# Optimization experiments

Measured on AMD Instinct MI355X. Metric: run time of the kernel, lower is better.

## Reference

```python
import jax, jax.numpy as jnp
import numpy as np
from jax import lax

PRE_NMS_TOPN = 2000
POST_NMS_TOPN = 1000
NMS_THRESH = 0.7
MIN_BOX_SIZE = 4.0
BBOX_XFORM_CLIP = 4.135  # log(1000/16), standard clamp on dw/dh


def setup_inputs() -> dict:
    key = jax.random.key(0)
    k1, k2, k3, k4 = jax.random.split(key, 4)
    B, N = 8, 250000
    H, W = 800, 1333
    rpn_bbox_pred = jax.random.normal(k1, (B, N, 4), jnp.float32) * 0.5
    objectness = jax.random.normal(k2, (B, N), jnp.float32)
    # realistic anchors: centers inside image, sizes in [16, 256]
    ctr = jax.random.uniform(k3, (N, 2), jnp.float32) * jnp.array([W, H], jnp.float32)
    wh = jax.random.uniform(k4, (N, 2), jnp.float32) * 240.0 + 16.0
    anchors = jnp.concatenate([ctr - 0.5 * wh, ctr + 0.5 * wh], axis=-1)
    return {"rpn_bbox_pred": rpn_bbox_pred, "objectness": objectness,
            "anchors": anchors, "height": H, "width": W}


def _decode_clip(anchors, deltas, height, width):
    # anchors (1,N,4) broadcast against deltas (B,N,4); boxes are x1,y1,x2,y2
    aw = anchors[..., 2] - anchors[..., 0]
    ah = anchors[..., 3] - anchors[..., 1]
    ax = anchors[..., 0] + 0.5 * aw
    ay = anchors[..., 1] + 0.5 * ah
    dx, dy = deltas[..., 0], deltas[..., 1]
    dw = jnp.minimum(deltas[..., 2], BBOX_XFORM_CLIP)
    dh = jnp.minimum(deltas[..., 3], BBOX_XFORM_CLIP)
    px = dx * aw + ax
    py = dy * ah + ay
    pw = jnp.exp(dw) * aw
    ph = jnp.exp(dh) * ah
    x1 = jnp.clip(px - 0.5 * pw, 0.0, float(width))
    y1 = jnp.clip(py - 0.5 * ph, 0.0, float(height))
    x2 = jnp.clip(px + 0.5 * pw, 0.0, float(width))
    y2 = jnp.clip(py + 0.5 * ph, 0.0, float(height))
    return jnp.stack([x1, y1, x2, y2], axis=-1)


def _pairwise_iou(boxes):
    # boxes (K,4) -> iou (K,K)
    x1, y1, x2, y2 = boxes[:, 0], boxes[:, 1], boxes[:, 2], boxes[:, 3]
    area = (x2 - x1) * (y2 - y1)
    iw = jnp.maximum(jnp.minimum(x2[:, None], x2[None, :]) - jnp.maximum(x1[:, None], x1[None, :]), 0.0)
    ih = jnp.maximum(jnp.minimum(y2[:, None], y2[None, :]) - jnp.maximum(y1[:, None], y1[None, :]), 0.0)
    inter = iw * ih
    return inter / (area[:, None] + area[None, :] - inter + 1e-9)


def _nms_keep(boxes, valid):
    # sequential greedy NMS over score-sorted boxes (K,4); returns keep mask (K,)
    iou = lax.stop_gradient(_pairwise_iou(boxes))
    idxs = jnp.arange(PRE_NMS_TOPN)
    def body(i, keep):
        sup = (iou[i] > NMS_THRESH) & keep[i] & (idxs > i)
        return keep & (~sup)
    return lax.fori_loop(0, PRE_NMS_TOPN, body, valid)


def _per_image(boxes, scores):
    # boxes (N,4), scores (N,)
    ws = boxes[:, 2] - boxes[:, 0]
    hs = boxes[:, 3] - boxes[:, 1]
    size_ok = (ws >= MIN_BOX_SIZE) & (hs >= MIN_BOX_SIZE)
    masked = jnp.where(size_ok, scores, -jnp.inf)
    top_s, order = lax.top_k(masked, PRE_NMS_TOPN)   # descending sort + pre-NMS topN
    top_boxes = boxes[order]                          # (PRE,4)
    valid = top_s > -jnp.inf                          # boxes surviving size filter
    keep = _nms_keep(top_boxes, valid)
    # take first POST_NMS_TOPN kept boxes in score order (fixed-shape padding)
    sel = jnp.sort(jnp.where(keep, jnp.arange(PRE_NMS_TOPN), PRE_NMS_TOPN))[:POST_NMS_TOPN]
    out_valid = sel < PRE_NMS_TOPN
    sel_c = jnp.minimum(sel, PRE_NMS_TOPN - 1)
    out = jnp.where(out_valid[:, None], top_boxes[sel_c], 0.0)
    return out, out_valid


def reference(rpn_bbox_pred, objectness, anchors, height, width):
    proposals = _decode_clip(anchors[None], rpn_bbox_pred, height, width)  # (B,N,4)
    out, valid = jax.vmap(_per_image)(proposals, objectness)
    # padded equivalent of the ragged per-image list: (B,POST,4) boxes + (B,POST) validity
    return out, valid
```

## Files before the change

### kernel.cpp

```cpp
#include <hip/hip_runtime.h>
#include <hip/hip_bf16.h>

#define NBUCK 8192
#define P1B   32
#define CAP   4096
#define TOPN  2000
#define NP2   2048
#define OUTN  1000
#define NST   64
#define NSLOT 8
#define SLOTW 2048

typedef unsigned int u32x4 __attribute__((ext_vector_type(4)));
typedef __attribute__((address_space(1))) const unsigned GUP;
typedef __attribute__((address_space(3))) unsigned LUP;

__device__ __forceinline__ float4 decode_box(const float4 a, const float4 d, float W, float H) {
    float aw = a.z - a.x;
    float ah = a.w - a.y;
    float ax = a.x + 0.5f * aw;
    float ay = a.y + 0.5f * ah;
    float dw = fminf(d.z, 4.135f);
    float dh = fminf(d.w, 4.135f);
    float px = d.x * aw + ax;
    float py = d.y * ah + ay;
    float pw = expf(dw) * aw;
    float ph = expf(dh) * ah;
    float4 r;
    r.x = fminf(fmaxf(px - 0.5f * pw, 0.0f), W);
    r.y = fminf(fmaxf(py - 0.5f * ph, 0.0f), H);
    r.z = fminf(fmaxf(px + 0.5f * pw, 0.0f), W);
    r.w = fminf(fmaxf(py + 0.5f * ph, 0.0f), H);
    return r;
}

__device__ __forceinline__ unsigned score_key(const float4 a, const float4 d, float W, float H, float s) {
    float4 b = decode_box(a, d, W, H);
    bool ok = ((b.z - b.x) >= 4.0f) && ((b.w - b.y) >= 4.0f);
    float ms = ok ? s : -INFINITY;
    unsigned u = __float_as_uint(ms);
    return (u & 0x80000000u) ? ~u : (u | 0x80000000u);
}

__global__ void __launch_bounds__(1024) k_pass1(const float* __restrict__ pred,
        const float* __restrict__ obj, const float* __restrict__ anch,
        const int* __restrict__ Hp, const int* __restrict__ Wp,
        unsigned* __restrict__ keys, unsigned* __restrict__ hist,
        unsigned* __restrict__ cnt, unsigned* __restrict__ remInit, int N) {
    __shared__ unsigned h[2 * NBUCK];
    int t = threadIdx.x;
    int b = blockIdx.y, g = blockIdx.x;
    if (g == 0 && t < 64) { if (t == 0) cnt[b * 64] = 0; remInit[b * 64 + t] = 0; }
    for (int i = t; i < 2 * NBUCK; i += 1024) h[i] = 0;
    __syncthreads();
    int chunk = (N + P1B - 1) / P1B;
    int base = g * chunk;
    int end = base + chunk; if (end > N) end = N;
    float W = (float)*Wp, H = (float)*Hp;
    unsigned cp = (t & 1) ? NBUCK : 0;
    for (int n = base + t; n < end; n += 1024) {
        float4 a = ((const float4*)anch)[n];
        float4 d = ((const float4*)pred)[(size_t)b * N + n];
        float s = obj[(size_t)b * N + n];
        unsigned key = score_key(a, d, W, H, s);
        keys[(size_t)b * N + n] = key;
        atomicAdd(&h[cp + (key >> 19)], 1u);
    }
    __syncthreads();
    for (int i = t; i < NBUCK; i += 1024) {
        unsigned v = h[i] + h[NBUCK + i];
        if (v) atomicAdd(&hist[b * NBUCK + i], v);
    }
}

__global__ void k_scan(const unsigned* __restrict__ hist, unsigned* __restrict__ Lb) {
    __shared__ unsigned h[NBUCK];
    __shared__ unsigned csum[256];
    __shared__ unsigned suf[256];
    __shared__ int tcS;
    __shared__ unsigned beforeS;
    int b = blockIdx.x, t = threadIdx.x;
    const unsigned* src = hist + (size_t)b * NBUCK;
    for (int i = t * 4; i < NBUCK; i += 1024) {
        uint4 v = *(const uint4*)(src + i);
        h[i] = v.x; h[i + 1] = v.y; h[i + 2] = v.z; h[i + 3] = v.w;
    }
    if (t == 0) tcS = -1;
    __syncthreads();
    unsigned s = 0;
    for (int j = 0; j < 32; j++) s += h[t * 32 + j];
    csum[t] = s; suf[t] = s;
    __syncthreads();
    for (int d = 1; d < 256; d <<= 1) {
        unsigned v = (t + d < 256) ? suf[t + d] : 0;
        __syncthreads();
        suf[t] += v;
        __syncthreads();
    }
    if (suf[t] >= (unsigned)TOPN && (t == 255 || suf[t + 1] < (unsigned)TOPN)) {
        tcS = t; beforeS = (t == 255) ? 0u : suf[t + 1];
    }
    __syncthreads();
    if (t == 0) {
        unsigned L = 0;
        int tc = tcS;
        if (tc >= 0) {
            unsigned r = beforeS;
            for (int bkt = tc * 32 + 31;; bkt--) {
                r += h[bkt];
                if (r >= (unsigned)TOPN || bkt == tc * 32) { L = (unsigned)bkt; break; }
            }
        }
        Lb[b] = L;
    }
}

__global__ void k_collect(const unsigned* __restrict__ keys, const unsigned* __restrict__ Lb,
                          unsigned* __restrict__ count, unsigned long long* __restrict__ cand,
                          int N) {
    __shared__ unsigned lk[1024], ln[1024];
    __shared__ unsigned lcnt, lbase;
    int b = blockIdx.y, t = threadIdx.x;
    if (t == 0) lcnt = 0;
    __syncthreads();
    unsigned L = Lb[b];
    const unsigned* kb = keys + (size_t)b * N;
    int e = blockIdx.x * 256 + t;
    int n0 = e * 4;
    if (n0 + 3 < N) {
        uint4 kv = ((const uint4*)kb)[e];
        if ((kv.x >> 19) >= L) { unsigned p = atomicAdd(&lcnt, 1u); lk[p] = kv.x; ln[p] = n0; }
        if ((kv.y >> 19) >= L) { unsigned p = atomicAdd(&lcnt, 1u); lk[p] = kv.y; ln[p] = n0 + 1; }
        if ((kv.z >> 19) >= L) { unsigned p = atomicAdd(&lcnt, 1u); lk[p] = kv.z; ln[p] = n0 + 2; }
        if ((kv.w >> 19) >= L) { unsigned p = atomicAdd(&lcnt, 1u); lk[p] = kv.w; ln[p] = n0 + 3; }
    } else {
        for (int j = 0; j < 4; j++) {
            int n = n0 + j;
            if (n < N) {
                unsigned k = kb[n];
                if ((k >> 19) >= L) { unsigned p = atomicAdd(&lcnt, 1u); lk[p] = k; ln[p] = n; }
            }
        }
    }
    __syncthreads();
    if (t == 0) lbase = atomicAdd(&count[b * 64], lcnt);
    __syncthreads();
    unsigned c = lcnt, bs = lbase;
    for (unsigned i = t; i < c; i += 256) {
        unsigned pos = bs + i;
        if (pos < CAP) cand[(size_t)b * CAP + pos] =
            ((unsigned long long)lk[i] << 32) | (unsigned)(~ln[i]);
    }
}

#define REGX(e, p, d, lo)  ((lo) == (d) ? ((e) >= (p) ? (e) : (p)) : ((e) >= (p) ? (p) : (e)))

__global__ void __launch_bounds__(256) k_sort1(unsigned long long* __restrict__ cand,
        const unsigned* __restrict__ count) {
    __shared__ unsigned long long s[512];
    int b = blockIdx.x >> 3, g = blockIdx.x & 7;
    int t = threadIdx.x;
    unsigned cnt = count[b * 64]; if (cnt > CAP) cnt = CAP;
    unsigned long long* cb = cand + (size_t)b * CAP + g * 512;
    int g0 = g * 512 + t, g1 = g * 512 + t + 256;
    unsigned long long e0 = (g0 < (int)cnt) ? cb[t] : 0ULL;
    unsigned long long e1 = (g1 < (int)cnt) ? cb[t + 256] : 0ULL;

    #pragma unroll
    for (int k = 2; k <= 64; k <<= 1) {
        bool d0 = ((g0 & k) == 0);
        bool d1 = ((g1 & k) == 0);
        #pragma unroll
        for (int j = k >> 1; j >= 1; j >>= 1) {
            bool lo = ((t & j) == 0);
            unsigned long long p0 = __shfl_xor(e0, j, 64);
            unsigned long long p1 = __shfl_xor(e1, j, 64);
            e0 = REGX(e0, p0, d0, lo);
            e1 = REGX(e1, p1, d1, lo);
        }
    }
    for (int k = 128; k <= 512; k <<= 1) {
        s[t] = e0; s[t + 256] = e1;
        __syncthreads();
        for (int j = k >> 1; j >= 64; j >>= 1) {
            int i = ((t & ~(j - 1)) << 1) | (t & (j - 1));
            int l = i + j;
            bool desc = (((g * 512 + i) & k) == 0);
            unsigned long long x = s[i], y = s[l];
            if (desc ? (x < y) : (x > y)) { s[i] = y; s[l] = x; }
            __syncthreads();
        }
        e0 = s[t]; e1 = s[t + 256];
        bool d0 = ((g0 & k) == 0);
        bool d1 = ((g1 & k) == 0);
        #pragma unroll
        for (int j = 32; j >= 1; j >>= 1) {
            bool lo = ((t & j) == 0);
            unsigned long long p0 = __shfl_xor(e0, j, 64);
            unsigned long long p1 = __shfl_xor(e1, j, 64);
            e0 = REGX(e0, p0, d0, lo);
            e1 = REGX(e1, p1, d1, lo);
        }
    }
    cb[t] = e0; cb[t + 256] = e1;
}

__global__ void __launch_bounds__(1024) k_sort2(const unsigned long long* __restrict__ cand,
        const float* __restrict__ pred, const float* __restrict__ anch,
        const int* __restrict__ Hp, const int* __restrict__ Wp,
        float4* __restrict__ topbox, unsigned* __restrict__ remInit, int N) {
    __shared__ unsigned long long s[CAP];
    int b = blockIdx.x, t = threadIdx.x;
    const unsigned long long* cb = cand + (size_t)b * CAP;
    unsigned long long e0 = cb[t], e1 = cb[t + 1024], e2 = cb[t + 2048], e3 = cb[t + 3072];
    for (int k = 1024; k <= 4096; k <<= 1) {
        s[t] = e0; s[t + 1024] = e1; s[t + 2048] = e2; s[t + 3072] = e3;
        __syncthreads();
        for (int j = k >> 1; j >= 64; j >>= 1) {
            #pragma unroll
            for (int cc = 0; cc < 2; cc++) {
                int c = t + cc * 1024;
                int i = ((c & ~(j - 1)) << 1) | (c & (j - 1));
                int l = i + j;
                bool desc = ((i & k) == 0);
                unsigned long long x = s[i], y = s[l];
                if (desc ? (x < y) : (x > y)) { s[i] = y; s[l] = x; }
            }
            __syncthreads();
        }
        e0 = s[t]; e1 = s[t + 1024]; e2 = s[t + 2048]; e3 = s[t + 3072];
        bool d0 = ((t & k) == 0);
        bool d1 = (((t + 1024) & k) == 0);
        bool d2 = (((t + 2048) & k) == 0);
        bool d3 = (((t + 3072) & k) == 0);
        #pragma unroll
        for (int j = 32; j >= 1; j >>= 1) {
            bool lo = ((t & j) == 0);
            unsigned long long p0 = __shfl_xor(e0, j, 64);
            unsigned long long p1 = __shfl_xor(e1, j, 64);
            unsigned long long p2 = __shfl_xor(e2, j, 64);
            unsigned long long p3 = __shfl_xor(e3, j, 64);
            e0 = REGX(e0, p0, d0, lo);
            e1 = REGX(e1, p1, d1, lo);
            e2 = REGX(e2, p2, d2, lo);
            e3 = REGX(e3, p3, d3, lo);
        }
    }
    float W = (float)*Wp, H = (float)*Hp;
    #pragma unroll
    for (int m = 0; m < 2; m++) {
        unsigned long long v = m ? e1 : e0;
        int r = t + m * 1024;
        unsigned key = (unsigned)(v >> 32);
        bool valid = key > 0x007FFFFFu;
        float4 outb = {0.f, 0.f, 0.f, 0.f};
        if (valid) {
            unsigned idx = ~((unsigned)v);
            float4 a = ((const float4*)anch)[idx];
            float4 d = ((const float4*)pred)[(size_t)b * N + idx];
            outb = decode_box(a, d, W, H);
        }
        topbox[(size_t)b * NP2 + r] = outb;
        if (r < TOPN && !valid) atomicOr(&remInit[b * 64 + (r >> 5)], 1u << (r & 31));
    }
}

__global__ void __launch_bounds__(256) k_mask(const float4* __restrict__ topbox,
                                              unsigned* __restrict__ maskT) {
    const double MID = 23488103.0 / 33554432.0;
    __shared__ float4 bx[NP2];
    __shared__ float ar[NP2];
    int b = blockIdx.y, c = blockIdx.x;
    int t = threadIdx.x;
    int j0 = c * 32;
    for (int i = j0 + t; i < NP2; i += 256) {
        float4 v = topbox[(size_t)b * NP2 + i];
        bx[i] = v;
        ar[i] = (v.z - v.x) * (v.w - v.y);
    }
    __syncthreads();
    int r = t & 31;
    int wg = t >> 5;
    int i = j0 + r;
    float4 bi = bx[i];
    float areai = ar[i];
    unsigned* outc = maskT + ((size_t)(b * NST + c)) * SLOTW;
    for (int w = wg; w < c; w += 8) outc[w * 32 + r] = 0u;
    for (int w = c + wg; w < 64; w += 8) {
        unsigned bits = 0;
        int jbase = w * 32;
        #pragma unroll
        for (int jj = 0; jj < 32; jj++) {
            int j = jbase + jj;
            float4 bj = bx[j];
            float iw = fmaxf(fminf(bi.z, bj.z) - fmaxf(bi.x, bj.x), 0.0f);
            float ih = fmaxf(fminf(bi.w, bj.w) - fmaxf(bi.y, bj.y), 0.0f);
            float inter = iw * ih;
            float denom = areai + ar[j] - inter + 1e-9f;
            if ((double)inter >= MID * (double)denom) bits |= (1u << jj);
        }
        if (w == c) bits &= ~((2u << r) - 1u);
        outc[w * 32 + r] = bits;
    }
}

__global__ void __launch_bounds__(512) k_nms(const unsigned* __restrict__ maskT,
        const unsigned* __restrict__ remInit, const float4* __restrict__ topbox,
        float* __restrict__ out, int B) {
    __shared__ __align__(16) unsigned smbuf[NSLOT * SLOTW];
    __shared__ int ready[NST];
    __shared__ int consumed;
    __shared__ int stop;
    int b = blockIdx.x;
    int t = threadIdx.x;
    const unsigned* m = maskT + (size_t)b * NST * SLOTW;

    float4* ob = (float4*)out + (size_t)b * OUTN;
    for (int i = t; i < OUTN; i += 512) ob[i] = make_float4(0.f, 0.f, 0.f, 0.f);
    float* vout = out + (size_t)B * (OUTN * 4) + (size_t)b * OUTN;
    for (int i = t; i < OUTN; i += 512) vout[i] = 0.0f;

    if (t < NST) ready[t] = 0;
    if (t == 0) { consumed = 0; stop = 0; }
    __syncthreads();

    unsigned removed = 0xFFFFFFFFu;

    if (t >= 64) {
        int w = t >> 6;
        int lam = t & 63;
        int base = ((lam >> 3) << 5) + ((((lam & 7) ^ ((lam >> 3) & 7))) << 2);
        #pragma unroll 1
        for (int s = w - 1; s < NST; s += 7) {
            if (__hip_atomic_load(&stop, __ATOMIC_RELAXED, __HIP_MEMORY_SCOPE_WORKGROUP)) break;
            while (__hip_atomic_load(&consumed, __ATOMIC_ACQUIRE,
                   __HIP_MEMORY_SCOPE_WORKGROUP) < s - (NSLOT - 1))
                __builtin_amdgcn_s_sleep(2);
            const unsigned* gs = m + (size_t)s * SLOTW + base;
            unsigned* sl = smbuf + (s & (NSLOT - 1)) * SLOTW;
            #pragma unroll
            for (int i = 0; i < 8; i++)
                __builtin_amdgcn_global_load_lds((GUP*)(gs + i * 256),
                                                 (LUP*)(sl + i * 256), 16, 0, 0);
            asm volatile("s_waitcnt vmcnt(0)" ::: "memory");
            if (lam == 0) __hip_atomic_store(&ready[s], 1, __ATOMIC_RELEASE,
                                             __HIP_MEMORY_SCOPE_WORKGROUP);
        }
    } else {
        removed = remInit[b * 64 + t];
        if (t == 62) removed |= 0xFFFF0000u;
        if (t == 63) removed = 0xFFFFFFFFu;
        int e = t & 7;
        int keptRun = 0;
        #pragma unroll 1
        for (int s = 0; s < NST; s++) {
            while (!__hip_atomic_load(&ready[s], __ATOMIC_ACQUIRE,
                   __HIP_MEMORY_SCOPE_WORKGROUP))
                __builtin_amdgcn_s_sleep(2);
            const u32x4* sq = (const u32x4*)(smbuf + (s & (NSLOT - 1)) * SLOTW) + t * 8;
            unsigned R[32];
            #pragma unroll
            for (int k = 0; k < 8; k++) *(u32x4*)&R[k << 2] = sq[k ^ e];
            __builtin_amdgcn_sched_group_barrier(0x100, 8, 0);
            unsigned alive = ~__builtin_amdgcn_readlane(removed, s);
            unsigned Is[32];
            #pragma unroll
            for (int q = 0; q < 32; q++) Is[q] = __builtin_amdgcn_readlane(R[q], s);
            #pragma unroll
            for (int q = 0; q < 32; q++) alive &= ~(((alive >> q) & 1u) ? Is[q] : 0u);
            unsigned a0 = 0, a1 = 0, a2 = 0, a3 = 0;
            #pragma unroll
            for (int q = 0; q < 32; q += 4) {
                a0 |= ((alive >> q) & 1u)       ? R[q]     : 0u;
                a1 |= ((alive >> (q + 1)) & 1u) ? R[q + 1] : 0u;
                a2 |= ((alive >> (q + 2)) & 1u) ? R[q + 2] : 0u;
                a3 |= ((alive >> (q + 3)) & 1u) ? R[q + 3] : 0u;
            }
            removed |= (a0 | a1) | (a2 | a3);
            keptRun += __popc(~__builtin_amdgcn_readlane(removed, s));
            if (keptRun >= OUTN) {
                if (t == 0) {
                    __hip_atomic_store(&stop, 1, __ATOMIC_RELAXED, __HIP_MEMORY_SCOPE_WORKGROUP);
                    __hip_atomic_store(&consumed, NST, __ATOMIC_RELEASE, __HIP_MEMORY_SCOPE_WORKGROUP);
                }
                break;
            }
            if (t == 0) __hip_atomic_store(&consumed, s + 1, __ATOMIC_RELEASE,
                                           __HIP_MEMORY_SCOPE_WORKGROUP);
        }
        unsigned keep = ~removed;
        int cnt = __popc(keep);
        int ex = cnt;
        for (int off = 1; off < 64; off <<= 1) {
            int v = __shfl_up(ex, off, 64);
            if (t >= off) ex += v;
        }
        ex -= cnt;
        int pos = ex;
        for (int j = 0; j < 32; j++) {
            if ((keep >> j) & 1u) {
                if (pos < OUTN) {
                    float4 bxv = topbox[(size_t)b * NP2 + t * 32 + j];
                    ob[pos] = bxv;
                    vout[pos] = 1.0f;
                }
                pos++;
            }
        }
    }
}

extern "C" void kernel_launch(void* const* d_in, const int* in_sizes, int n_in,
                              void* d_out, int out_size, void* d_ws, size_t ws_size,
                              hipStream_t stream) {
    const float* pred = (const float*)d_in[0];
    const float* obj  = (const float*)d_in[1];
    const float* anch = (const float*)d_in[2];
    const int* Hp = (const int*)d_in[3];
    const int* Wp = (const int*)d_in[4];
    int N = in_sizes[2] / 4;
    int B = in_sizes[1] / N;

    char* ws = (char*)d_ws;
    size_t off = 0;
    auto take = [&](size_t bytes) { void* p = ws + off; off = (off + bytes + 255) & ~(size_t)255; return p; };

    size_t regA_bytes = (size_t)B * N * 4;
    size_t mask_bytes = (size_t)B * NST * SLOTW * 4;
    char* regA = (char*)take(regA_bytes > mask_bytes ? regA_bytes : mask_bytes);
    unsigned* keys  = (unsigned*)regA;
    unsigned* maskT = (unsigned*)regA;
    unsigned* hist           = (unsigned*)take((size_t)B * NBUCK * 4);
    unsigned long long* cand = (unsigned long long*)take((size_t)B * CAP * 8);
    float4* topbox           = (float4*)take((size_t)B * NP2 * 16);
    unsigned* cnt            = (unsigned*)take((size_t)B * 64 * 4);
    unsigned* Lb             = (unsigned*)take((size_t)B * 64 * 4);
    unsigned* remInit        = (unsigned*)take((size_t)B * 64 * 4);

    hipMemsetAsync(hist, 0, (size_t)B * NBUCK * 4, stream);

    k_pass1  <<<dim3(P1B, B), 1024, 0, stream>>>(pred, obj, anch, Hp, Wp, keys, hist, cnt, remInit, N);
    k_scan   <<<B, 256, 0, stream>>>(hist, Lb);
    k_collect<<<dim3((N + 1023) / 1024, B), 256, 0, stream>>>(keys, Lb, cnt, cand, N);
    k_sort1  <<<B * 8, 256, 0, stream>>>(cand, cnt);
    k_sort2  <<<B, 1024, 0, stream>>>(cand, pred, anch, Hp, Wp, topbox, remInit, N);
    k_mask   <<<dim3(NST, B), 256, 0, stream>>>(topbox, maskT);
    k_nms    <<<B, 512, 0, stream>>>(maskT, remInit, topbox, (float*)d_out, B);
}
```

Measured before the change: 123.4 us.

## Fuse all pipeline stages into one persistent kernel with software grid barriers

Replaces the seven separate kernel launches (plus memset) with one persistent kernel of 240 blocks. The blocks step through histogram, threshold scan, collect, two sort stages, mask build and NMS, separated by atomic-counter grid barriers. A small zeroing kernel replaces the memset and also clears the counters, remInit and barrier state. The aim is to remove launch and inter-kernel gap overhead. The cost is that many stages leave most blocks idle, the barrier relies on all 240 blocks being co-resident, and the mask stage now keeps 32 of 64 row words per block per pass.

After: 288.9 us. +134.1%, slower.

```diff
diff --git a/kernel.cpp b/kernel.cpp
--- a/kernel.cpp
+++ b/kernel.cpp
@@ -2,7 +2,8 @@
 #include <hip/hip_bf16.h>
 
 #define NBUCK 8192
-#define P1B   32
+#define NBLK  240
+#define PIMG  30
 #define CAP   4096
 #define TOPN  2000
 #define NP2   2048
@@ -10,6 +11,7 @@
 #define NST   64
 #define NSLOT 8
 #define SLOTW 2048
+#define ZWORDS (2*NBUCK*4 + 512 + 512 + 64)
 
 typedef unsigned int u32x4 __attribute__((ext_vector_type(4)));
 typedef __attribute__((address_space(1))) const unsigned GUP;
@@ -42,369 +44,417 @@
     return (u & 0x80000000u) ? ~u : (u | 0x80000000u);
 }
 
-__global__ void __launch_bounds__(1024) k_pass1(const float* __restrict__ pred,
-        const float* __restrict__ obj, const float* __restrict__ anch,
-        const int* __restrict__ Hp, const int* __restrict__ Wp,
-        unsigned* __restrict__ keys, unsigned* __restrict__ hist,
-        unsigned* __restrict__ cnt, unsigned* __restrict__ remInit, int N) {
-    __shared__ unsigned h[2 * NBUCK];
+__global__ void k_zero(unsigned* __restrict__ p, int nq) {
+    int i = blockIdx.x * 256 + threadIdx.x;
+    if (i < nq) ((u32x4*)p)[i] = (u32x4){0u, 0u, 0u, 0u};
+}
+
+__device__ __forceinline__ void gridbar(unsigned* bar, int cell) {
+    __syncthreads();
+    if (threadIdx.x == 0) {
+        unsigned* c = bar + cell * 2;
+        unsigned* g = bar + cell * 2 + 1;
+        __threadfence();
+        unsigned g0 = __hip_atomic_load(g, __ATOMIC_RELAXED, __HIP_MEMORY_SCOPE_AGENT);
+        unsigned a = __hip_atomic_fetch_add(c, 1u, __ATOMIC_ACQ_REL, __HIP_MEMORY_SCOPE_AGENT);
+        if (a == NBLK - 1) {
+            __hip_atomic_store(c, 0u, __ATOMIC_RELAXED, __HIP_MEMORY_SCOPE_AGENT);
+            __hip_atomic_store(g, g0 + 1u, __ATOMIC_RELEASE, __HIP_MEMORY_SCOPE_AGENT);
+        } else {
+            while (__hip_atomic_load(g, __ATOMIC_ACQUIRE, __HIP_MEMORY_SCOPE_AGENT) == g0)
+                __builtin_amdgcn_s_sleep(8);
+        }
+        __threadfence();
+    }
+    __syncthreads();
+}
+
+#define REGX(e, p, d, lo)  ((lo) == (d) ? ((e) >= (p) ? (e) : (p)) : ((e) >= (p) ? (p) : (e)))
+
+__global__ void __launch_bounds__(1024) k_mega(
+        const float* __restrict__ pred, const float* __restrict__ obj,
+        const float* __restrict__ anch, const int* __restrict__ Hp,
+        const int* __restrict__ Wp, unsigned* __restrict__ keys,
+        unsigned* __restrict__ hist, unsigned* __restrict__ cntg,
+        unsigned* __restrict__ remInit, unsigned* __restrict__ Lb,
+        unsigned long long* __restrict__ cand, float4* __restrict__ topbox,
+        unsigned* __restrict__ maskT, float* __restrict__ out,
+        unsigned* __restrict__ bar, int N, int B) {
+    __shared__ __align__(16) char Lraw[65808];
+    int bid = blockIdx.x;
     int t = threadIdx.x;
-    int b = blockIdx.y, g = blockIdx.x;
-    if (g == 0 && t < 64) { if (t == 0) cnt[b * 64] = 0; remInit[b * 64 + t] = 0; }
-    for (int i = t; i < 2 * NBUCK; i += 1024) h[i] = 0;
-    __syncthreads();
-    int chunk = (N + P1B - 1) / P1B;
-    int base = g * chunk;
-    int end = base + chunk; if (end > N) end = N;
     float W = (float)*Wp, H = (float)*Hp;
-    unsigned cp = (t & 1) ? NBUCK : 0;
-    for (int n = base + t; n < end; n += 1024) {
-        float4 a = ((const float4*)anch)[n];
-        float4 d = ((const float4*)pred)[(size_t)b * N + n];
-        float s = obj[(size_t)b * N + n];
-        unsigned key = score_key(a, d, W, H, s);
-        keys[(size_t)b * N + n] = key;
-        atomicAdd(&h[cp + (key >> 19)], 1u);
-    }
-    __syncthreads();
-    for (int i = t; i < NBUCK; i += 1024) {
-        unsigned v = h[i] + h[NBUCK + i];
-        if (v) atomicAdd(&hist[b * NBUCK + i], v);
-    }
-}
-
-__global__ void k_scan(const unsigned* __restrict__ hist, unsigned* __restrict__ Lb) {
-    __shared__ unsigned h[NBUCK];
-    __shared__ unsigned csum[256];
-    __shared__ unsigned suf[256];
-    __shared__ int tcS;
-    __shared__ unsigned beforeS;
-    int b = blockIdx.x, t = threadIdx.x;
-    const unsigned* src = hist + (size_t)b * NBUCK;
-    for (int i = t * 4; i < NBUCK; i += 1024) {
-        uint4 v = *(const uint4*)(src + i);
-        h[i] = v.x; h[i + 1] = v.y; h[i + 2] = v.z; h[i + 3] = v.w;
-    }
-    if (t == 0) tcS = -1;
-    __syncthreads();
-    unsigned s = 0;
-    for (int j = 0; j < 32; j++) s += h[t * 32 + j];
-    csum[t] = s; suf[t] = s;
-    __syncthreads();
-    for (int d = 1; d < 256; d <<= 1) {
-        unsigned v = (t + d < 256) ? suf[t + d] : 0;
-        __syncthreads();
-        suf[t] += v;
-        __syncthreads();
-    }
-    if (suf[t] >= (unsigned)TOPN && (t == 255 || suf[t + 1] < (unsigned)TOPN)) {
-        tcS = t; beforeS = (t == 255) ? 0u : suf[t + 1];
-    }
-    __syncthreads();
-    if (t == 0) {
-        unsigned L = 0;
-        int tc = tcS;
-        if (tc >= 0) {
-            unsigned r = beforeS;
-            for (int bkt = tc * 32 + 31;; bkt--) {
-                r += h[bkt];
-                if (r >= (unsigned)TOPN || bkt == tc * 32) { L = (unsigned)bkt; break; }
-            }
-        }
-        Lb[b] = L;
-    }
-}
-
-__global__ void k_collect(const unsigned* __restrict__ keys, const unsigned* __restrict__ Lb,
-                          unsigned* __restrict__ count, unsigned long long* __restrict__ cand,
-                          int N) {
-    __shared__ unsigned lk[1024], ln[1024];
-    __shared__ unsigned lcnt, lbase;
-    int b = blockIdx.y, t = threadIdx.x;
-    if (t == 0) lcnt = 0;
-    __syncthreads();
-    unsigned L = Lb[b];
-    const unsigned* kb = keys + (size_t)b * N;
-    int e = blockIdx.x * 256 + t;
-    int n0 = e * 4;
-    if (n0 + 3 < N) {
-        uint4 kv = ((const uint4*)kb)[e];
-        if ((kv.x >> 19) >= L) { unsigned p = atomicAdd(&lcnt, 1u); lk[p] = kv.x; ln[p] = n0; }
-        if ((kv.y >> 19) >= L) { unsigned p = atomicAdd(&lcnt, 1u); lk[p] = kv.y; ln[p] = n0 + 1; }
-        if ((kv.z >> 19) >= L) { unsigned p = atomicAdd(&lcnt, 1u); lk[p] = kv.z; ln[p] = n0 + 2; }
-        if ((kv.w >> 19) >= L) { unsigned p = atomicAdd(&lcnt, 1u); lk[p] = kv.w; ln[p] = n0 + 3; }
-    } else {
-        for (int j = 0; j < 4; j++) {
-            int n = n0 + j;
-            if (n < N) {
-                unsigned k = kb[n];
-                if ((k >> 19) >= L) { unsigned p = atomicAdd(&lcnt, 1u); lk[p] = k; ln[p] = n; }
-            }
-        }
-    }
-    __syncthreads();
-    if (t == 0) lbase = atomicAdd(&count[b * 64], lcnt);
-    __syncthreads();
-    unsigned c = lcnt, bs = lbase;
-    for (unsigned i = t; i < c; i += 256) {
-        unsigned pos = bs + i;
-        if (pos < CAP) cand[(size_t)b * CAP + pos] =
-            ((unsigned long long)lk[i] << 32) | (unsigned)(~ln[i]);
-    }
-}
-
-#define REGX(e, p, d, lo)  ((lo) == (d) ? ((e) >= (p) ? (e) : (p)) : ((e) >= (p) ? (p) : (e)))
-
-__global__ void __launch_bounds__(256) k_sort1(unsigned long long* __restrict__ cand,
-        const unsigned* __restrict__ count) {
-    __shared__ unsigned long long s[512];
-    int b = blockIdx.x >> 3, g = blockIdx.x & 7;
-    int t = threadIdx.x;
-    unsigned cnt = count[b * 64]; if (cnt > CAP) cnt = CAP;
-    unsigned long long* cb = cand + (size_t)b * CAP + g * 512;
-    int g0 = g * 512 + t, g1 = g * 512 + t + 256;
-    unsigned long long e0 = (g0 < (int)cnt) ? cb[t] : 0ULL;
-    unsigned long long e1 = (g1 < (int)cnt) ? cb[t + 256] : 0ULL;
-
-    #pragma unroll
-    for (int k = 2; k <= 64; k <<= 1) {
-        bool d0 = ((g0 & k) == 0);
-        bool d1 = ((g1 & k) == 0);
+
+    {
+        unsigned* h = (unsigned*)Lraw;
+        int b = bid / PIMG, g = bid % PIMG;
+        for (int i = t; i < 2 * NBUCK; i += 1024) h[i] = 0;
+        __syncthreads();
+        int chunk = (N + PIMG - 1) / PIMG;
+        int base = g * chunk;
+        int end = base + chunk; if (end > N) end = N;
+        unsigned cp = (t & 1) ? NBUCK : 0;
+        for (int n = base + t; n < end; n += 1024) {
+            float4 a = ((const float4*)anch)[n];
+            float4 d = ((const float4*)pred)[(size_t)b * N + n];
+            float s = obj[(size_t)b * N + n];
+            unsigned key = score_key(a, d, W, H, s);
+            keys[(size_t)b * N + n] = key;
+            atomicAdd(&h[cp + (key >> 19)], 1u);
+        }
+        __syncthreads();
+        for (int i = t; i < NBUCK; i += 1024) {
+            unsigned v = h[i] + h[NBUCK + i];
+            if (v) atomicAdd(&hist[b * NBUCK + i], v);
+        }
+    }
+    gridbar(bar, 0);
+
+    if (bid < B) {
+        unsigned* h1   = (unsigned*)Lraw;
+        unsigned* csum = (unsigned*)(Lraw + 32768);
+        unsigned* suf  = (unsigned*)(Lraw + 33792);
+        int* tcS       = (int*)(Lraw + 34816);
+        unsigned* befS = (unsigned*)(Lraw + 34820);
+        int b = bid;
+        const unsigned* src = hist + (size_t)b * NBUCK;
+        for (int i = t * 4; i < NBUCK; i += 4096) {
+            uint4 v = *(const uint4*)(src + i);
+            h1[i] = v.x; h1[i + 1] = v.y; h1[i + 2] = v.z; h1[i + 3] = v.w;
+        }
+        if (t == 0) *tcS = -1;
+        __syncthreads();
+        if (t < 256) {
+            unsigned s = 0;
+            for (int j = 0; j < 32; j++) s += h1[t * 32 + j];
+            csum[t] = s; suf[t] = s;
+        }
+        __syncthreads();
+        for (int d = 1; d < 256; d <<= 1) {
+            unsigned v = (t < 256 && t + d < 256) ? suf[t + d] : 0;
+            __syncthreads();
+            if (t < 256) suf[t] += v;
+            __syncthreads();
+        }
+        if (t < 256 && suf[t] >= (unsigned)TOPN && (t == 255 || suf[t + 1] < (unsigned)TOPN)) {
+            *tcS = t; *befS = (t == 255) ? 0u : suf[t + 1];
+        }
+        __syncthreads();
+        if (t == 0) {
+            unsigned L = 0;
+            int tc = *tcS;
+            if (tc >= 0) {
+                unsigned r = *befS;
+                for (int bkt = tc * 32 + 31;; bkt--) {
+                    r += h1[bkt];
+                    if (r >= (unsigned)TOPN || bkt == tc * 32) { L = (unsigned)bkt; break; }
+                }
+            }
+            Lb[b] = L;
+        }
+    }
+    gridbar(bar, 1);
+
+    {
+        unsigned* lk    = (unsigned*)Lraw;
+        unsigned* ln    = (unsigned*)(Lraw + 16384);
+        unsigned* lcnt  = (unsigned*)(Lraw + 32768);
+        unsigned* lbase = (unsigned*)(Lraw + 32784);
+        int b = bid / PIMG, g = bid % PIMG;
+        int grp = t >> 8, lt = t & 255;
+        const unsigned* kb = keys + (size_t)b * N;
+        unsigned Lth = Lb[b];
+        int V = N >> 2;
+        int SUBT = (V + 255) >> 8;
+        for (int it = 0; it < 3; it++) {
+            int st = g * 4 + grp + (PIMG * 4) * it;
+            if (lt == 0) lcnt[grp] = 0;
+            __syncthreads();
+            bool act = st < SUBT;
+            if (act) {
+                int e = st * 256 + lt;
+                if (e < V) {
+                    uint4 kv = ((const uint4*)kb)[e];
+                    int n0 = e * 4;
+                    if ((kv.x >> 19) >= Lth) { unsigned p = atomicAdd(&lcnt[grp], 1u); lk[grp * 1024 + p] = kv.x; ln[grp * 1024 + p] = n0; }
+                    if ((kv.y >> 19) >= Lth) { unsigned p = atomicAdd(&lcnt[grp], 1u); lk[grp * 1024 + p] = kv.y; ln[grp * 1024 + p] = n0 + 1; }
+                    if ((kv.z >> 19) >= Lth) { unsigned p = atomicAdd(&lcnt[grp], 1u); lk[grp * 1024 + p] = kv.z; ln[grp * 1024 + p] = n0 + 2; }
+                    if ((kv.w >> 19) >= Lth) { unsigned p = atomicAdd(&lcnt[grp], 1u); lk[grp * 1024 + p] = kv.w; ln[grp * 1024 + p] = n0 + 3; }
+                }
+            }
+            __syncthreads();
+            if (act && lt == 0) lbase[grp] = atomicAdd(&cntg[b * 64], lcnt[grp]);
+            __syncthreads();
+            if (act) {
+                unsigned c2 = lcnt[grp], bs = lbase[grp];
+                for (unsigned i2 = lt; i2 < c2; i2 += 256) {
+                    unsigned pos = bs + i2;
+                    if (pos < CAP) cand[(size_t)b * CAP + pos] =
+                        ((unsigned long long)lk[grp * 1024 + i2] << 32) | (unsigned)(~ln[grp * 1024 + i2]);
+                }
+            }
+            __syncthreads();
+        }
+    }
+    gridbar(bar, 2);
+
+    if (bid < 64) {
+        unsigned long long* s1 = (unsigned long long*)Lraw;
+        int b = bid >> 3, g = bid & 7;
+        unsigned cnt = cntg[b * 64]; if (cnt > CAP) cnt = CAP;
+        unsigned long long* cb = cand + (size_t)b * CAP + g * 512;
+        int g0 = g * 512 + t, g1 = g * 512 + t + 256;
+        unsigned long long e0 = 0, e1 = 0;
+        if (t < 256) {
+            e0 = (g0 < (int)cnt) ? cb[t] : 0ULL;
+            e1 = (g1 < (int)cnt) ? cb[t + 256] : 0ULL;
+            #pragma unroll
+            for (int k = 2; k <= 64; k <<= 1) {
+                bool d0 = ((g0 & k) == 0);
+                bool d1 = ((g1 & k) == 0);
+                #pragma unroll
+                for (int j = k >> 1; j >= 1; j >>= 1) {
+                    bool lo = ((t & j) == 0);
+                    unsigned long long p0 = __shfl_xor(e0, j, 64);
+                    unsigned long long p1 = __shfl_xor(e1, j, 64);
+                    e0 = REGX(e0, p0, d0, lo);
+                    e1 = REGX(e1, p1, d1, lo);
+                }
+            }
+        }
+        for (int k = 128; k <= 512; k <<= 1) {
+            if (t < 256) { s1[t] = e0; s1[t + 256] = e1; }
+            __syncthreads();
+            for (int j = k >> 1; j >= 64; j >>= 1) {
+                if (t < 256) {
+                    int i = ((t & ~(j - 1)) << 1) | (t & (j - 1));
+                    int l = i + j;
+                    bool desc = (((g * 512 + i) & k) == 0);
+                    unsigned long long x = s1[i], y = s1[l];
+                    if (desc ? (x < y) : (x > y)) { s1[i] = y; s1[l] = x; }
+                }
+                __syncthreads();
+            }
+            if (t < 256) {
+                e0 = s1[t]; e1 = s1[t + 256];
+                bool d0 = ((g0 & k) == 0);
+                bool d1 = ((g1 & k) == 0);
+                #pragma unroll
+                for (int j = 32; j >= 1; j >>= 1) {
+                    bool lo = ((t & j) == 0);
+                    unsigned long long p0 = __shfl_xor(e0, j, 64);
+                    unsigned long long p1 = __shfl_xor(e1, j, 64);
+                    e0 = REGX(e0, p0, d0, lo);
+                    e1 = REGX(e1, p1, d1, lo);
+                }
+            }
+        }
+        if (t < 256) { cb[t] = e0; cb[t + 256] = e1; }
+    }
+    gridbar(bar, 3);
+
+    if (bid < B) {
+        unsigned long long* s = (unsigned long long*)Lraw;
+        int b = bid;
+        const unsigned long long* cb = cand + (size_t)b * CAP;
+        unsigned long long e0 = cb[t], e1 = cb[t + 1024], e2 = cb[t + 2048], e3 = cb[t + 3072];
+        for (int k = 1024; k <= 4096; k <<= 1) {
+            s[t] = e0; s[t + 1024] = e1; s[t + 2048] = e2; s[t + 3072] = e3;
+            __syncthreads();
+            for (int j = k >> 1; j >= 64; j >>= 1) {
+                #pragma unroll
+                for (int cc = 0; cc < 2; cc++) {
+                    int c = t + cc * 1024;
+                    int i = ((c & ~(j - 1)) << 1) | (c & (j - 1));
+                    int l = i + j;
+                    bool desc = ((i & k) == 0);
+                    unsigned long long x = s[i], y = s[l];
+                    if (desc ? (x < y) : (x > y)) { s[i] = y; s[l] = x; }
+                }
+                __syncthreads();
+            }
+            e0 = s[t]; e1 = s[t + 1024]; e2 = s[t + 2048]; e3 = s[t + 3072];
+            bool d0 = ((t & k) == 0);
+            bool d1 = (((t + 1024) & k) == 0);
+            bool d2 = (((t + 2048) & k) == 0);
+            bool d3 = (((t + 3072) & k) == 0);
+            #pragma unroll
+            for (int j = 32; j >= 1; j >>= 1) {
+                bool lo = ((t & j) == 0);
+                unsigned long long p0 = __shfl_xor(e0, j, 64);
+                unsigned long long p1 = __shfl_xor(e1, j, 64);
+                unsigned long long p2 = __shfl_xor(e2, j, 64);
+                unsigned long long p3 = __shfl_xor(e3, j, 64);
+                e0 = REGX(e0, p0, d0, lo);
+                e1 = REGX(e1, p1, d1, lo);
+                e2 = REGX(e2, p2, d2, lo);
+                e3 = REGX(e3, p3, d3, lo);
+            }
+        }
         #pragma unroll
-        for (int j = k >> 1; j >= 1; j >>= 1) {
-            bool lo = ((t & j) == 0);
-            unsigned long long p0 = __shfl_xor(e0, j, 64);
-            unsigned long long p1 = __shfl_xor(e1, j, 64);
-            e0 = REGX(e0, p0, d0, lo);
-            e1 = REGX(e1, p1, d1, lo);
-        }
-    }
-    for (int k = 128; k <= 512; k <<= 1) {
-        s[t] = e0; s[t + 256] = e1;
-        __syncthreads();
-        for (int j = k >> 1; j >= 64; j >>= 1) {
-            int i = ((t & ~(j - 1)) << 1) | (t & (j - 1));
-            int l = i + j;
-            bool desc = (((g * 512 + i) & k) == 0);
-            unsigned long long x = s[i], y = s[l];
-            if (desc ? (x < y) : (x > y)) { s[i] = y; s[l] = x; }
-            __syncthreads();
-        }
-        e0 = s[t]; e1 = s[t + 256];
-        bool d0 = ((g0 & k) == 0);
-        bool d1 = ((g1 & k) == 0);
-        #pragma unroll
-        for (int j = 32; j >= 1; j >>= 1) {
-            bool lo = ((t & j) == 0);
-            unsigned long long p0 = __shfl_xor(e0, j, 64);
-            unsigned long long p1 = __shfl_xor(e1, j, 64);
-            e0 = REGX(e0, p0, d0, lo);
-            e1 = REGX(e1, p1, d1, lo);
-        }
-    }
-    cb[t] = e0; cb[t + 256] = e1;
-}
-
-__global__ void __launch_bounds__(1024) k_sort2(const unsigned long long* __restrict__ cand,
-        const float* __restrict__ pred, const float* __restrict__ anch,
-        const int* __restrict__ Hp, const int* __restrict__ Wp,
-        float4* __restrict__ topbox, unsigned* __restrict__ remInit, int N) {
-    __shared__ unsigned long long s[CAP];
-    int b = blockIdx.x, t = threadIdx.x;
-    const unsigned long long* cb = cand + (size_t)b * CAP;
-    unsigned long long e0 = cb[t], e1 = cb[t + 1024], e2 = cb[t + 2048], e3 = cb[t + 3072];
-    for (int k = 1024; k <= 4096; k <<= 1) {
-        s[t] = e0; s[t + 1024] = e1; s[t + 2048] = e2; s[t + 3072] = e3;
-        __syncthreads();
-        for (int j = k >> 1; j >= 64; j >>= 1) {
-            #pragma unroll
-            for (int cc = 0; cc < 2; cc++) {
-                int c = t + cc * 1024;
-                int i = ((c & ~(j - 1)) << 1) | (c & (j - 1));
-                int l = i + j;
-                bool desc = ((i & k) == 0);
-                unsigned long long x = s[i], y = s[l];
-                if (desc ? (x < y) : (x > y)) { s[i] = y; s[l] = x; }
-            }
-            __syncthreads();
-        }
-        e0 = s[t]; e1 = s[t + 1024]; e2 = s[t + 2048]; e3 = s[t + 3072];
-        bool d0 = ((t & k) == 0);
-        bool d1 = (((t + 1024) & k) == 0);
-        bool d2 = (((t + 2048) & k) == 0);
-        bool d3 = (((t + 3072) & k) == 0);
-        #pragma unroll
-        for (int j = 32; j >= 1; j >>= 1) {
-            bool lo = ((t & j) == 0);
-            unsigned long long p0 = __shfl_xor(e0, j, 64);
-            unsigned long long p1 = __shfl_xor(e1, j, 64);
-            unsigned long long p2 = __shfl_xor(e2, j, 64);
-            unsigned long long p3 = __shfl_xor(e3, j, 64);
-            e0 = REGX(e0, p0, d0, lo);
-            e1 = REGX(e1, p1, d1, lo);
-            e2 = REGX(e2, p2, d2, lo);
-            e3 = REGX(e3, p3, d3, lo);
-        }
-    }
-    float W = (float)*Wp, H = (float)*Hp;
-    #pragma unroll
-    for (int m = 0; m < 2; m++) {
-        unsigned long long v = m ? e1 : e0;
-        int r = t + m * 1024;
-        unsigned key = (unsigned)(v >> 32);
-        bool valid = key > 0x007FFFFFu;
-        float4 outb = {0.f, 0.f, 0.f, 0.f};
-        if (valid) {
-            unsigned idx = ~((unsigned)v);
-            float4 a = ((const float4*)anch)[idx];
-            float4 d = ((const float4*)pred)[(size_t)b * N + idx];
-            outb = decode_box(a, d, W, H);
-        }
-        topbox[(size_t)b * NP2 + r] = outb;
-        if (r < TOPN && !valid) atomicOr(&remInit[b * 64 + (r >> 5)], 1u << (r & 31));
-    }
-}
-
-__global__ void __launch_bounds__(256) k_mask(const float4* __restrict__ topbox,
-                                              unsigned* __restrict__ maskT) {
-    const double MID = 23488103.0 / 33554432.0;
-    __shared__ float4 bx[NP2];
-    __shared__ float ar[NP2];
-    int b = blockIdx.y, c = blockIdx.x;
-    int t = threadIdx.x;
-    int j0 = c * 32;
-    for (int i = j0 + t; i < NP2; i += 256) {
-        float4 v = topbox[(size_t)b * NP2 + i];
-        bx[i] = v;
-        ar[i] = (v.z - v.x) * (v.w - v.y);
-    }
-    __syncthreads();
-    int r = t & 31;
-    int wg = t >> 5;
-    int i = j0 + r;
-    float4 bi = bx[i];
-    float areai = ar[i];
-    unsigned* outc = maskT + ((size_t)(b * NST + c)) * SLOTW;
-    for (int w = wg; w < c; w += 8) outc[w * 32 + r] = 0u;
-    for (int w = c + wg; w < 64; w += 8) {
-        unsigned bits = 0;
-        int jbase = w * 32;
-        #pragma unroll
-        for (int jj = 0; jj < 32; jj++) {
-            int j = jbase + jj;
-            float4 bj = bx[j];
-            float iw = fmaxf(fminf(bi.z, bj.z) - fmaxf(bi.x, bj.x), 0.0f);
-            float ih = fmaxf(fminf(bi.w, bj.w) - fmaxf(bi.y, bj.y), 0.0f);
-            float inter = iw * ih;
-            float denom = areai + ar[j] - inter + 1e-9f;
-            if ((double)inter >= MID * (double)denom) bits |= (1u << jj);
-        }
-        if (w == c) bits &= ~((2u << r) - 1u);
-        outc[w * 32 + r] = bits;
-    }
-}
-
-__global__ void __launch_bounds__(512) k_nms(const unsigned* __restrict__ maskT,
-        const unsigned* __restrict__ remInit, const float4* __restrict__ topbox,
-        float* __restrict__ out, int B) {
-    __shared__ __align__(16) unsigned smbuf[NSLOT * SLOTW];
-    __shared__ int ready[NST];
-    __shared__ int consumed;
-    __shared__ int stop;
-    int b = blockIdx.x;
-    int t = threadIdx.x;
-    const unsigned* m = maskT + (size_t)b * NST * SLOTW;
-
-    float4* ob = (float4*)out + (size_t)b * OUTN;
-    for (int i = t; i < OUTN; i += 512) ob[i] = make_float4(0.f, 0.f, 0.f, 0.f);
-    float* vout = out + (size_t)B * (OUTN * 4) + (size_t)b * OUTN;
-    for (int i = t; i < OUTN; i += 512) vout[i] = 0.0f;
-
-    if (t < NST) ready[t] = 0;
-    if (t == 0) { consumed = 0; stop = 0; }
-    __syncthreads();
-
-    unsigned removed = 0xFFFFFFFFu;
-
-    if (t >= 64) {
-        int w = t >> 6;
-        int lam = t & 63;
-        int base = ((lam >> 3) << 5) + ((((lam & 7) ^ ((lam >> 3) & 7))) << 2);
-        #pragma unroll 1
-        for (int s = w - 1; s < NST; s += 7) {
-            if (__hip_atomic_load(&stop, __ATOMIC_RELAXED, __HIP_MEMORY_SCOPE_WORKGROUP)) break;
-            while (__hip_atomic_load(&consumed, __ATOMIC_ACQUIRE,
-                   __HIP_MEMORY_SCOPE_WORKGROUP) < s - (NSLOT - 1))
-                __builtin_amdgcn_s_sleep(2);
-            const unsigned* gs = m + (size_t)s * SLOTW + base;
-            unsigned* sl = smbuf + (s & (NSLOT - 1)) * SLOTW;
-            #pragma unroll
-            for (int i = 0; i < 8; i++)
-                __builtin_amdgcn_global_load_lds((GUP*)(gs + i * 256),
-                                                 (LUP*)(sl + i * 256), 16, 0, 0);
-            asm volatile("s_waitcnt vmcnt(0)" ::: "memory");
-            if (lam == 0) __hip_atomic_store(&ready[s], 1, __ATOMIC_RELEASE,
-                                             __HIP_MEMORY_SCOPE_WORKGROUP);
-        }
-    } else {
-        removed = remInit[b * 64 + t];
-        if (t == 62) removed |= 0xFFFF0000u;
-        if (t == 63) removed = 0xFFFFFFFFu;
-        int e = t & 7;
-        int keptRun = 0;
-        #pragma unroll 1
-        for (int s = 0; s < NST; s++) {
-            while (!__hip_atomic_load(&ready[s], __ATOMIC_ACQUIRE,
-                   __HIP_MEMORY_SCOPE_WORKGROUP))
-                __builtin_amdgcn_s_sleep(2);
-            const u32x4* sq = (const u32x4*)(smbuf + (s & (NSLOT - 1)) * SLOTW) + t * 8;
-            unsigned R[32];
-            #pragma unroll
-            for (int k = 0; k < 8; k++) *(u32x4*)&R[k << 2] = sq[k ^ e];
-            __builtin_amdgcn_sched_group_barrier(0x100, 8, 0);
-            unsigned alive = ~__builtin_amdgcn_readlane(removed, s);
-            unsigned Is[32];
-            #pragma unroll
-            for (int q = 0; q < 32; q++) Is[q] = __builtin_amdgcn_readlane(R[q], s);
-            #pragma unroll
-            for (int q = 0; q < 32; q++) alive &= ~(((alive >> q) & 1u) ? Is[q] : 0u);
-            unsigned a0 = 0, a1 = 0, a2 = 0, a3 = 0;
-            #pragma unroll
-            for (int q = 0; q < 32; q += 4) {
-                a0 |= ((alive >> q) & 1u)       ? R[q]     : 0u;
-                a1 |= ((alive >> (q + 1)) & 1u) ? R[q + 1] : 0u;
-                a2 |= ((alive >> (q + 2)) & 1u) ? R[q + 2] : 0u;
-                a3 |= ((alive >> (q + 3)) & 1u) ? R[q + 3] : 0u;
-            }
-            removed |= (a0 | a1) | (a2 | a3);
-            keptRun += __popc(~__builtin_amdgcn_readlane(removed, s));
-            if (keptRun >= OUTN) {
-                if (t == 0) {
-                    __hip_atomic_store(&stop, 1, __ATOMIC_RELAXED, __HIP_MEMORY_SCOPE_WORKGROUP);
-                    __hip_atomic_store(&consumed, NST, __ATOMIC_RELEASE, __HIP_MEMORY_SCOPE_WORKGROUP);
-                }
-                break;
-            }
-            if (t == 0) __hip_atomic_store(&consumed, s + 1, __ATOMIC_RELEASE,
-                                           __HIP_MEMORY_SCOPE_WORKGROUP);
-        }
-        unsigned keep = ~removed;
-        int cnt = __popc(keep);
-        int ex = cnt;
-        for (int off = 1; off < 64; off <<= 1) {
-            int v = __shfl_up(ex, off, 64);
-            if (t >= off) ex += v;
-        }
-        ex -= cnt;
-        int pos = ex;
-        for (int j = 0; j < 32; j++) {
-            if ((keep >> j) & 1u) {
-                if (pos < OUTN) {
-                    float4 bxv = topbox[(size_t)b * NP2 + t * 32 + j];
-                    ob[pos] = bxv;
-                    vout[pos] = 1.0f;
-                }
-                pos++;
+        for (int m = 0; m < 2; m++) {
+            unsigned long long v = m ? e1 : e0;
+            int r = t + m * 1024;
+            unsigned key = (unsigned)(v >> 32);
+            bool valid = key > 0x007FFFFFu;
+            float4 outb = {0.f, 0.f, 0.f, 0.f};
+            if (valid) {
+                unsigned idx = ~((unsigned)v);
+                float4 a = ((const float4*)anch)[idx];
+                float4 d = ((const float4*)pred)[(size_t)b * N + idx];
+                outb = decode_box(a, d, W, H);
+            }
+            topbox[(size_t)b * NP2 + r] = outb;
+            if (r < TOPN && !valid) atomicOr(&remInit[b * 64 + (r >> 5)], 1u << (r & 31));
+        }
+    }
+    gridbar(bar, 4);
+
+    {
+        const double MID = 23488103.0 / 33554432.0;
+        float4* bx = (float4*)Lraw;
+        float*  ar = (float*)(Lraw + 32768);
+        for (int it = 0; it < 3; it++) {
+            int task = bid + it * NBLK;
+            bool act = task < 8 * NST;
+            int mb = task >> 6, c = task & 63;
+            int j0 = c * 32;
+            if (act) {
+                for (int i = j0 + t; i < NP2; i += 1024) {
+                    float4 v = topbox[(size_t)mb * NP2 + i];
+                    bx[i] = v;
+                    ar[i] = (v.z - v.x) * (v.w - v.y);
+                }
+            }
+            __syncthreads();
+            if (act) {
+                int r = t & 31;
+                int wg = t >> 5;
+                int i = j0 + r;
+                float4 bi = bx[i];
+                float areai = ar[i];
+                unsigned* outc = maskT + ((size_t)(mb * NST + c)) * SLOTW;
+                for (int w = wg; w < 64; w += 32) {
+                    if (w < c) { outc[w * 32 + r] = 0u; continue; }
+                    unsigned bits = 0;
+                    int jbase = w * 32;
+                    #pragma unroll
+                    for (int jj = 0; jj < 32; jj++) {
+                        int j = jbase + jj;
+                        float4 bj = bx[j];
+                        float iw = fmaxf(fminf(bi.z, bj.z) - fmaxf(bi.x, bj.x), 0.0f);
+                        float ih = fmaxf(fminf(bi.w, bj.w) - fmaxf(bi.y, bj.y), 0.0f);
+                        float inter = iw * ih;
+                        float denom = areai + ar[j] - inter + 1e-9f;
+                        if ((double)inter >= MID * (double)denom) bits |= (1u << jj);
+                    }
+                    if (w == c) bits &= ~((2u << r) - 1u);
+                    outc[w * 32 + r] = bits;
+                }
+            }
+            __syncthreads();
+        }
+    }
+    gridbar(bar, 5);
+
+    if (bid < B) {
+        unsigned* smbuf = (unsigned*)Lraw;
+        int* ready      = (int*)(Lraw + 65536);
+        int* consumed   = (int*)(Lraw + 65792);
+        int* stop       = (int*)(Lraw + 65796);
+        int b = bid;
+        const unsigned* m = maskT + (size_t)b * NST * SLOTW;
+
+        float4* ob = (float4*)out + (size_t)b * OUTN;
+        for (int i = t; i < OUTN; i += 1024) ob[i] = make_float4(0.f, 0.f, 0.f, 0.f);
+        float* vout = out + (size_t)B * (OUTN * 4) + (size_t)b * OUTN;
+        for (int i = t; i < OUTN; i += 1024) vout[i] = 0.0f;
+
+        if (t < NST) ready[t] = 0;
+        if (t == 0) { *consumed = 0; *stop = 0; }
+        __syncthreads();
+
+        if (t >= 512) {
+        } else if (t >= 64) {
+            int w = t >> 6;
+            int lam = t & 63;
+            int base = ((lam >> 3) << 5) + ((((lam & 7) ^ ((lam >> 3) & 7))) << 2);
+            #pragma unroll 1
+            for (int s = w - 1; s < NST; s += 7) {
+                if (__hip_atomic_load(stop, __ATOMIC_RELAXED, __HIP_MEMORY_SCOPE_WORKGROUP)) break;
+                while (__hip_atomic_load(consumed, __ATOMIC_ACQUIRE,
+                       __HIP_MEMORY_SCOPE_WORKGROUP) < s - (NSLOT - 1))
+                    __builtin_amdgcn_s_sleep(2);
+                const unsigned* gs = m + (size_t)s * SLOTW + base;
+                unsigned* sl = smbuf + (s & (NSLOT - 1)) * SLOTW;
+                #pragma unroll
+                for (int i = 0; i < 8; i++)
+                    __builtin_amdgcn_global_load_lds((GUP*)(gs + i * 256),
+                                                     (LUP*)(sl + i * 256), 16, 0, 0);
+                asm volatile("s_waitcnt vmcnt(0)" ::: "memory");
+                if (lam == 0) __hip_atomic_store(&ready[s], 1, __ATOMIC_RELEASE,
+                                                 __HIP_MEMORY_SCOPE_WORKGROUP);
+            }
+        } else {
+            unsigned removed = remInit[b * 64 + t];
+            if (t == 62) removed |= 0xFFFF0000u;
+            if (t == 63) removed = 0xFFFFFFFFu;
+            int e = t & 7;
+            int keptRun = 0;
+            #pragma unroll 1
+            for (int s = 0; s < NST; s++) {
+                while (!__hip_atomic_load(&ready[s], __ATOMIC_ACQUIRE,
+                       __HIP_MEMORY_SCOPE_WORKGROUP))
+                    __builtin_amdgcn_s_sleep(2);
+                const u32x4* sq = (const u32x4*)(smbuf + (s & (NSLOT - 1)) * SLOTW) + t * 8;
+                unsigned R[32];
+                #pragma unroll
+                for (int k = 0; k < 8; k++) *(u32x4*)&R[k << 2] = sq[k ^ e];
+                __builtin_amdgcn_sched_group_barrier(0x100, 8, 0);
+                unsigned alive = ~__builtin_amdgcn_readlane(removed, s);
+                unsigned Is[32];
+                #pragma unroll
+                for (int q = 0; q < 32; q++) Is[q] = __builtin_amdgcn_readlane(R[q], s);
+                #pragma unroll
+                for (int q = 0; q < 32; q++) alive &= ~(((alive >> q) & 1u) ? Is[q] : 0u);
+                unsigned a0 = 0, a1 = 0, a2 = 0, a3 = 0;
+                #pragma unroll
+                for (int q = 0; q < 32; q += 4) {
+                    a0 |= ((alive >> q) & 1u)       ? R[q]     : 0u;
+                    a1 |= ((alive >> (q + 1)) & 1u) ? R[q + 1] : 0u;
+                    a2 |= ((alive >> (q + 2)) & 1u) ? R[q + 2] : 0u;
+                    a3 |= ((alive >> (q + 3)) & 1u) ? R[q + 3] : 0u;
+                }
+                removed |= (a0 | a1) | (a2 | a3);
+                keptRun += __popc(~__builtin_amdgcn_readlane(removed, s));
+                if (keptRun >= OUTN) {
+                    if (t == 0) {
+                        __hip_atomic_store(stop, 1, __ATOMIC_RELAXED, __HIP_MEMORY_SCOPE_WORKGROUP);
+                        __hip_atomic_store(consumed, NST, __ATOMIC_RELEASE, __HIP_MEMORY_SCOPE_WORKGROUP);
+                    }
+                    break;
+                }
+                if (t == 0) __hip_atomic_store(consumed, s + 1, __ATOMIC_RELEASE,
+                                               __HIP_MEMORY_SCOPE_WORKGROUP);
+            }
+            unsigned keep = ~removed;
+            int cnt = __popc(keep);
+            int ex = cnt;
+            for (int off = 1; off < 64; off <<= 1) {
+                int v = __shfl_up(ex, off, 64);
+                if (t >= off) ex += v;
+            }
+            ex -= cnt;
+            int pos = ex;
+            for (int j = 0; j < 32; j++) {
+                if ((keep >> j) & 1u) {
+                    if (pos < OUTN) {
+                        float4 bxv = topbox[(size_t)b * NP2 + t * 32 + j];
+                        ob[pos] = bxv;
+                        vout[pos] = 1.0f;
+                    }
+                    pos++;
+                }
             }
         }
     }
@@ -430,20 +480,18 @@
     char* regA = (char*)take(regA_bytes > mask_bytes ? regA_bytes : mask_bytes);
     unsigned* keys  = (unsigned*)regA;
     unsigned* maskT = (unsigned*)regA;
-    unsigned* hist           = (unsigned*)take((size_t)B * NBUCK * 4);
+    unsigned* zr      = (unsigned*)take((size_t)ZWORDS * 4);
+    unsigned* hist    = zr;
+    unsigned* cntg    = zr + 2 * NBUCK * 4;
+    unsigned* remInit = cntg + 512;
+    unsigned* bar     = remInit + 512;
+    unsigned* Lb      = (unsigned*)take((size_t)B * 64 * 4);
     unsigned long long* cand = (unsigned long long*)take((size_t)B * CAP * 8);
     float4* topbox           = (float4*)take((size_t)B * NP2 * 16);
-    unsigned* cnt            = (unsigned*)take((size_t)B * 64 * 4);
-    unsigned* Lb             = (unsigned*)take((size_t)B * 64 * 4);
-    unsigned* remInit        = (unsigned*)take((size_t)B * 64 * 4);
-
-    hipMemsetAsync(hist, 0, (size_t)B * NBUCK * 4, stream);
-
-    k_pass1  <<<dim3(P1B, B), 1024, 0, stream>>>(pred, obj, anch, Hp, Wp, keys, hist, cnt, remInit, N);
-    k_scan   <<<B, 256, 0, stream>>>(hist, Lb);
-    k_collect<<<dim3((N + 1023) / 1024, B), 256, 0, stream>>>(keys, Lb, cnt, cand, N);
-    k_sort1  <<<B * 8, 256, 0, stream>>>(cand, cnt);
-    k_sort2  <<<B, 1024, 0, stream>>>(cand, pred, anch, Hp, Wp, topbox, remInit, N);
-    k_mask   <<<dim3(NST, B), 256, 0, stream>>>(topbox, maskT);
-    k_nms    <<<B, 512, 0, stream>>>(maskT, remInit, topbox, (float*)d_out, B);
-}
+
+    int nq = ZWORDS / 4;
+    k_zero<<<(nq + 255) / 256, 256, 0, stream>>>(zr, nq);
+    k_mega<<<NBLK, 1024, 0, stream>>>(pred, obj, anch, Hp, Wp, keys, hist, cntg,
+                                      remInit, Lb, cand, topbox, maskT,
+                                      (float*)d_out, bar, N, B);
+}
```
